# Kernel tuning notes

Hardware: AMD Instinct MI355X
Metric: run time of the kernel (lower is better)

Reference implementation:

```python
import jax, jax.numpy as jnp
import numpy as np

# TT config (matches init_kwargs)
NUM_TABLES = 4
P = (100, 100, 100)          # tt_p_shapes, prod = num_embeddings = 1e6
Q = (4, 4, 4)                # tt_q_shapes, prod = embedding_dim = 64
R = (1, 32, 32, 1)           # tt_ranks with boundary ranks
BAGS_PER_TABLE = 8192
POOL = 16                    # indices per bag


def setup_inputs() -> dict:
    key = jax.random.key(0)
    k1, k2, k3, k4 = jax.random.split(key, 4)
    nnz = NUM_TABLES * BAGS_PER_TABLE * POOL      # 524288
    B = NUM_TABLES * BAGS_PER_TABLE               # 32768 bags total
    indices = jax.random.randint(k1, (nnz,), 0, P[0] * P[1] * P[2], dtype=jnp.int64)
    offsets = (jnp.arange(B + 1, dtype=jnp.int64) * POOL)
    scale = 0.05  # small init, akin to approx-normal weight_dist
    tt_core_0 = jax.random.normal(k2, (NUM_TABLES, P[0], R[0] * Q[0] * R[1]), dtype=jnp.float32) * scale
    tt_core_1 = jax.random.normal(k3, (NUM_TABLES, P[1], R[1] * Q[1] * R[2]), dtype=jnp.float32) * scale
    tt_core_2 = jax.random.normal(k4, (NUM_TABLES, P[2], R[2] * Q[2] * R[3]), dtype=jnp.float32) * scale
    return {"indices": indices, "offsets": offsets,
            "tt_core_0": tt_core_0, "tt_core_1": tt_core_1, "tt_core_2": tt_core_2}


def reference(indices, offsets, tt_core_0, tt_core_1, tt_core_2):
    nnz = indices.shape[0]
    B = offsets.shape[0] - 1
    bags_per_table = B // NUM_TABLES

    # bag id for each nonzero (embedding-bag semantics), then table id per nonzero
    rowidx = jnp.searchsorted(offsets, jnp.arange(nnz, dtype=offsets.dtype), side='right') - 1
    tableidx = rowidx // bags_per_table

    # decompose flat row index into TT indices (C-order over p-shapes,
    # matching tt_matrix_to_full row layout)
    i0 = indices // (P[1] * P[2])
    i1 = (indices // P[2]) % P[1]
    i2 = indices % P[2]

    # gather per-lookup core slices
    c0 = tt_core_0[tableidx, i0].reshape(nnz, Q[0], R[1])          # r0 == 1
    c1 = tt_core_1[tableidx, i1].reshape(nnz, R[1], Q[1], R[2])
    c2 = tt_core_2[tableidx, i2].reshape(nnz, R[2], Q[2])          # r3 == 1

    # on-the-fly TT contraction to reconstruct embedding rows [nnz, D]
    t = jnp.einsum('nar,nrbs->nabs', c0, c1)                       # [nnz, q0, q1, r2]
    rows = jnp.einsum('nabs,nsc->nabc', t, c2).reshape(nnz, Q[0] * Q[1] * Q[2])

    # sum-pool per bag
    out = jax.ops.segment_sum(rows, rowidx, num_segments=B)        # [B, D]
    return out
```

## Files before the change

kernel.cpp:

```cpp
#include <hip/hip_runtime.h>
#include <stdint.h>

#define NT 4
#define PP 100
#define TT_BYTES (4ull * 100 * 100 * 1024)
#define C2B_DWORDS (NT * PP * 64)


typedef short bf16x8 __attribute__((ext_vector_type(8)));
typedef float f32x4  __attribute__((ext_vector_type(4)));

__device__ __forceinline__ uint32_t f2bf(float f) {
    union { float f; uint32_t u; } v; v.f = f;
    uint32_t u = v.u;
    return (u + 0x7fffu + ((u >> 16) & 1u)) >> 16;
}

__global__ __launch_bounds__(256)
void c2pack_kernel(const float* __restrict__ c2g, uint32_t* __restrict__ c2p) {
    int t = blockIdx.x * 256 + threadIdx.x;
    if (t >= C2B_DWORDS) return;
    int sg = t & 15, c = (t >> 4) & 3, combo = t >> 6;
    const float* src = c2g + (size_t)combo * 128;
    c2p[t] = f2bf(src[(2 * sg) * 4 + c]) | (f2bf(src[(2 * sg + 1) * 4 + c]) << 16);
}

__global__ __launch_bounds__(128, 3)
void tt_phase1(const float* __restrict__ c0g, const float* __restrict__ c1g,
               unsigned short* __restrict__ tT) {
    __shared__ float c1s[32 * 128];
    __shared__ float c0t[16 * 132];

    int blk = blockIdx.x;
    int tab   = blk / 700;
    int rem   = blk % 700;
    int i1    = rem / 7;
    int chunk = rem % 7;
    int i0_base = chunk * 16;
    int tid = threadIdx.x;

    const float4* c1p = (const float4*)(c1g + (size_t)(tab * PP + i1) * 4096);
    float4* c1v = (float4*)c1s;
    #pragma unroll
    for (int it = 0; it < 8; ++it) c1v[tid + 128 * it] = c1p[tid + 128 * it];

    #pragma unroll
    for (int it = 0; it < 16; ++it) {
        int f = tid + 128 * it;
        int i0l = f >> 7;
        int x   = f & 127;
        int a = x >> 5, r = x & 31;
        int i0 = i0_base + i0l; if (i0 > PP - 1) i0 = PP - 1;
        c0t[i0l * 132 + r * 4 + a] = c0g[(size_t)(tab * PP + i0) * 128 + x];
    }
    __syncthreads();

    int u  = tid >> 4;
    int sg = tid & 15;

    float acc[2][2][16];
    #pragma unroll
    for (int ii = 0; ii < 2; ++ii)
        #pragma unroll
        for (int e = 0; e < 2; ++e)
            #pragma unroll
            for (int q = 0; q < 16; ++q) acc[ii][e][q] = 0.f;

    #pragma unroll 4
    for (int r = 0; r < 32; ++r) {
        float4 av0 = *(const float4*)&c0t[(2 * u) * 132 + r * 4];
        float4 av1 = *(const float4*)&c0t[(2 * u + 1) * 132 + r * 4];
        const float* a0 = (const float*)&av0;
        const float* a1 = (const float*)&av1;
        #pragma unroll
        for (int b = 0; b < 4; ++b) {
            float2 bv = *(const float2*)&c1s[r * 128 + b * 32 + 2 * sg];
            #pragma unroll
            for (int a = 0; a < 4; ++a) {
                acc[0][0][a * 4 + b] += a0[a] * bv.x;
                acc[0][1][a * 4 + b] += a0[a] * bv.y;
                acc[1][0][a * 4 + b] += a1[a] * bv.x;
                acc[1][1][a * 4 + b] += a1[a] * bv.y;
            }
        }
    }

    #pragma unroll
    for (int ii = 0; ii < 2; ++ii) {
        int i0 = i0_base + 2 * u + ii;
        if (i0 >= PP) continue;
        size_t combo = (size_t)tab * 10000 + (size_t)i0 * 100 + (size_t)i1;
        char* base = (char*)tT + combo * 1024 + (size_t)sg * 4;
        #pragma unroll
        for (int ab = 0; ab < 16; ++ab) {
            uint32_t w = f2bf(acc[ii][0][ab]) | (f2bf(acc[ii][1][ab]) << 16);
            *(uint32_t*)(base + ab * 64) = w;
        }
    }
}

__global__ __launch_bounds__(256, 4)
void tt_phase2(const int* __restrict__ indices, const int* __restrict__ offsets,
               const char* __restrict__ tT, const char* __restrict__ c2b,
               float* __restrict__ out, int bags_per_table, int B) {
    int lane = threadIdx.x & 63;
    int wv   = threadIdx.x >> 6;
    int bag  = blockIdx.x * 4 + wv;
    if (bag >= B) return;
    int col = lane & 15;
    int kq  = lane >> 4;
    int tab = bag / bags_per_table;
    int start = offsets[bag];

    uint32_t idx = (uint32_t)indices[start + col];
    uint32_t i0 = idx / 10000u;
    uint32_t r1 = idx - i0 * 10000u;
    uint32_t i1 = r1 / 100u;
    uint32_t i2 = r1 - i1 * 100u;
    uint32_t tby = (((uint32_t)tab * 10000u + i0 * 100u + i1) << 10);
    uint32_t cby = (((uint32_t)tab * 100u + i2) << 8);

    int aoff = col * 64 + kq * 16;
    int boff = (col & 3) * 64 + kq * 16;

    bf16x8 A[16];
    #pragma unroll
    for (int j = 0; j < 16; ++j) {
        uint32_t tb = (uint32_t)__builtin_amdgcn_readlane((int)tby, j);
        A[j] = *(const bf16x8*)(tT + tb + aoff);
    }

    f32x4 acc = {0.f, 0.f, 0.f, 0.f};
    #pragma unroll
    for (int j = 0; j < 16; ++j) {
        uint32_t cb = (uint32_t)__builtin_amdgcn_readlane((int)cby, j);
        const bf16x8 Bv = *(const bf16x8*)(c2b + cb + boff);
        acc = __builtin_amdgcn_mfma_f32_16x16x32_bf16(A[j], Bv, acc, 0, 0, 0);
    }

    if (col < 4) {
        float* o = out + (size_t)bag * 64 + kq * 16 + col;
        o[0]  = acc[0];
        o[4]  = acc[1];
        o[8]  = acc[2];
        o[12] = acc[3];
    }
}

extern "C" void kernel_launch(void* const* d_in, const int* in_sizes, int n_in,
                              void* d_out, int out_size, void* d_ws, size_t ws_size,
                              hipStream_t stream) {
    const int*   indices = (const int*)d_in[0];
    const int*   offsets = (const int*)d_in[1];
    const float* c0      = (const float*)d_in[2];
    const float* c1      = (const float*)d_in[3];
    const float* c2      = (const float*)d_in[4];
    float* out = (float*)d_out;

    int B = in_sizes[1] - 1;
    int bags_per_table = B / NT;

    unsigned short* tT  = (unsigned short*)d_ws;
    uint32_t*       c2p = (uint32_t*)((char*)d_ws + TT_BYTES);

    c2pack_kernel<<<dim3((C2B_DWORDS + 255) / 256), dim3(256), 0, stream>>>(c2, c2p);
    tt_phase1<<<dim3(NT * PP * 7), dim3(128), 0, stream>>>(c0, c1, tT);
    tt_phase2<<<dim3((B + 3) / 4), dim3(256), 0, stream>>>(indices, offsets,
                                                           (const char*)tT,
                                                           (const char*)c2p, out,
                                                           bags_per_table, B);
}
```

Measured before the change: 158.0 us.

## Split each bag across four waves with LDS reduction; pack phase1 FMAs

Phase2 now assigns one block per bag, with each of four waves handling four lookups via four MFMAs and the partial results summed through shared memory. The aim is to expose more memory-level parallelism per bag and cut per-wave register pressure, allowing higher occupancy. It adds a block sync, an LDS reduction and four times as many blocks. Phase1 accumulators become float2 vectors so the compiler can emit packed FMA instructions.

After: 154.2 us. -2.4%, faster.

```diff
diff --git a/kernel.cpp b/kernel.cpp
--- a/kernel.cpp
+++ b/kernel.cpp
@@ -9,6 +9,7 @@
 
 typedef short bf16x8 __attribute__((ext_vector_type(8)));
 typedef float f32x4  __attribute__((ext_vector_type(4)));
+typedef float f32x2  __attribute__((ext_vector_type(2)));
 
 __device__ __forceinline__ uint32_t f2bf(float f) {
     union { float f; uint32_t u; } v; v.f = f;
@@ -58,13 +59,11 @@
     int u  = tid >> 4;
     int sg = tid & 15;
 
-    float acc[2][2][16];
+    f32x2 acc[2][16];
     #pragma unroll
     for (int ii = 0; ii < 2; ++ii)
         #pragma unroll
-        for (int e = 0; e < 2; ++e)
-            #pragma unroll
-            for (int q = 0; q < 16; ++q) acc[ii][e][q] = 0.f;
+        for (int q = 0; q < 16; ++q) acc[ii][q] = (f32x2){0.f, 0.f};
 
     #pragma unroll 4
     for (int r = 0; r < 32; ++r) {
@@ -74,13 +73,11 @@
         const float* a1 = (const float*)&av1;
         #pragma unroll
         for (int b = 0; b < 4; ++b) {
-            float2 bv = *(const float2*)&c1s[r * 128 + b * 32 + 2 * sg];
+            f32x2 bv = *(const f32x2*)&c1s[r * 128 + b * 32 + 2 * sg];
             #pragma unroll
             for (int a = 0; a < 4; ++a) {
-                acc[0][0][a * 4 + b] += a0[a] * bv.x;
-                acc[0][1][a * 4 + b] += a0[a] * bv.y;
-                acc[1][0][a * 4 + b] += a1[a] * bv.x;
-                acc[1][1][a * 4 + b] += a1[a] * bv.y;
+                acc[0][a * 4 + b] += (f32x2){a0[a], a0[a]} * bv;
+                acc[1][a * 4 + b] += (f32x2){a1[a], a1[a]} * bv;
             }
         }
     }
@@ -93,26 +90,26 @@
         char* base = (char*)tT + combo * 1024 + (size_t)sg * 4;
         #pragma unroll
         for (int ab = 0; ab < 16; ++ab) {
-            uint32_t w = f2bf(acc[ii][0][ab]) | (f2bf(acc[ii][1][ab]) << 16);
+            uint32_t w = f2bf(acc[ii][ab].x) | (f2bf(acc[ii][ab].y) << 16);
             *(uint32_t*)(base + ab * 64) = w;
         }
     }
 }
 
-__global__ __launch_bounds__(256, 4)
+__global__ __launch_bounds__(256, 6)
 void tt_phase2(const int* __restrict__ indices, const int* __restrict__ offsets,
                const char* __restrict__ tT, const char* __restrict__ c2b,
                float* __restrict__ out, int bags_per_table, int B) {
+    __shared__ float red[4][64];
     int lane = threadIdx.x & 63;
     int wv   = threadIdx.x >> 6;
-    int bag  = blockIdx.x * 4 + wv;
-    if (bag >= B) return;
+    int bag  = blockIdx.x;
     int col = lane & 15;
     int kq  = lane >> 4;
     int tab = bag / bags_per_table;
     int start = offsets[bag];
 
-    uint32_t idx = (uint32_t)indices[start + col];
+    uint32_t idx = (uint32_t)indices[start + wv * 4 + (col & 3)];
     uint32_t i0 = idx / 10000u;
     uint32_t r1 = idx - i0 * 10000u;
     uint32_t i1 = r1 / 100u;
@@ -123,27 +120,29 @@
     int aoff = col * 64 + kq * 16;
     int boff = (col & 3) * 64 + kq * 16;
 
-    bf16x8 A[16];
+    bf16x8 A[4], Bv[4];
     #pragma unroll
-    for (int j = 0; j < 16; ++j) {
-        uint32_t tb = (uint32_t)__builtin_amdgcn_readlane((int)tby, j);
-        A[j] = *(const bf16x8*)(tT + tb + aoff);
+    for (int jj = 0; jj < 4; ++jj) {
+        uint32_t tb = (uint32_t)__builtin_amdgcn_readlane((int)tby, jj);
+        uint32_t cb = (uint32_t)__builtin_amdgcn_readlane((int)cby, jj);
+        A[jj]  = *(const bf16x8*)(tT  + tb + aoff);
+        Bv[jj] = *(const bf16x8*)(c2b + cb + boff);
     }
 
     f32x4 acc = {0.f, 0.f, 0.f, 0.f};
     #pragma unroll
-    for (int j = 0; j < 16; ++j) {
-        uint32_t cb = (uint32_t)__builtin_amdgcn_readlane((int)cby, j);
-        const bf16x8 Bv = *(const bf16x8*)(c2b + cb + boff);
-        acc = __builtin_amdgcn_mfma_f32_16x16x32_bf16(A[j], Bv, acc, 0, 0, 0);
-    }
+    for (int jj = 0; jj < 4; ++jj)
+        acc = __builtin_amdgcn_mfma_f32_16x16x32_bf16(A[jj], Bv[jj], acc, 0, 0, 0);
 
     if (col < 4) {
-        float* o = out + (size_t)bag * 64 + kq * 16 + col;
-        o[0]  = acc[0];
-        o[4]  = acc[1];
-        o[8]  = acc[2];
-        o[12] = acc[3];
+        #pragma unroll
+        for (int q = 0; q < 4; ++q)
+            red[wv][kq * 16 + q * 4 + col] = acc[q];
+    }
+    __syncthreads();
+    if (wv == 0) {
+        float s = red[0][lane] + red[1][lane] + red[2][lane] + red[3][lane];
+        out[(size_t)bag * 64 + lane] = s;
     }
 }
 
@@ -165,8 +164,8 @@
 
     c2pack_kernel<<<dim3((C2B_DWORDS + 255) / 256), dim3(256), 0, stream>>>(c2, c2p);
     tt_phase1<<<dim3(NT * PP * 7), dim3(128), 0, stream>>>(c0, c1, tT);
-    tt_phase2<<<dim3((B + 3) / 4), dim3(256), 0, stream>>>(indices, offsets,
-                                                           (const char*)tT,
-                                                           (const char*)c2p, out,
-                                                           bags_per_table, B);
+    tt_phase2<<<dim3(B), dim3(256), 0, stream>>>(indices, offsets,
+                                                 (const char*)tT,
+                                                 (const char*)c2p, out,
+                                                 bags_per_table, B);
 }
```
